# Kernel tuning notes

Measured on AMD Instinct MI355X. Metric: run time of the kernel, lower is better.

## Reference

```python
import jax, jax.numpy as jnp
import numpy as np

N = 50000      # node_size
D = 256        # node_F == rel_F (ent_F)
R = 1000       # rel_size
E = 300000     # triple_size == n_edges
DEPTH = 2
KSEL = E // 2  # rows rewritten by W_orth transform
NPROXY = 128


def l2n(x):
    # tf.nn.l2_normalize with eps=1e-12
    return x * jax.lax.rsqrt(jnp.maximum(jnp.sum(x * x, axis=-1, keepdims=True), 1e-12))


def setup_inputs() -> dict:
    key = jax.random.key(0)
    ks = jax.random.split(key, 12)
    features = jax.random.normal(ks[0], (N, D), jnp.float32)
    rel_emb = jax.random.normal(ks[1], (R, D), jnp.float32)
    p = jax.random.normal(ks[2], (N, 1), jnp.float32)            # dynamic_node_kernel
    w_keys = jax.random.normal(ks[3], (DEPTH, D, D), jnp.float32) / np.float32(np.sqrt(D))
    attn_kernels = jax.random.normal(ks[4], (DEPTH, D, 1), jnp.float32) * 0.1
    proxy = jax.random.normal(ks[5], (NPROXY, D * (DEPTH + 1)), jnp.float32) * 0.05
    gate_kernel = jax.random.normal(ks[6], (D * (DEPTH + 1), D * (DEPTH + 1)), jnp.float32) / np.float32(np.sqrt(D * (DEPTH + 1)))
    adj_row = jnp.sort(jax.random.randint(ks[7], (E,), 0, N))    # destination (segment) ids, sorted
    adj_col = jax.random.randint(ks[8], (E,), 0, N)              # neighbor ids
    rel_ids = jax.random.randint(ks[9], (E,), 0, R)              # relation id per triple/edge
    rel_vals = jax.random.uniform(ks[10], (E,), jnp.float32)     # sparse_val per triple
    new_indices = jax.random.randint(ks[11], (KSEL,), 0, E)      # rows updated by w_key
    return dict(features=features, rel_emb=rel_emb, p=p, w_keys=w_keys,
                attn_kernels=attn_kernels, proxy=proxy, gate_kernel=gate_kernel,
                rel_vals=rel_vals, adj_row=adj_row, adj_col=adj_col,
                rel_ids=rel_ids, new_indices=new_indices)


def reference(features, rel_emb, p, w_keys, attn_kernels, proxy, gate_kernel,
              rel_vals, adj_row, adj_col, rel_ids, new_indices):
    tanh_p = jnp.tanh(p)                                   # [N,1]
    feats = features * tanh_p                              # use_p scaling (activation=None -> identity)
    outputs = [feats]
    for l in range(DEPTH):
        # sparse (triple,rel) x rel_emb : one relation per triple -> gather + scale
        rels_sum = rel_vals[:, None] * rel_emb[rel_ids]    # [E,D]
        rels_sum = l2n(rels_sum)
        # W_orth: transform a subset of rows by w_key, scatter back
        src = rels_sum[new_indices] @ w_keys[l]            # [KSEL,D]
        rels_sum = rels_sum.at[new_indices].set(src)
        neighs = feats[adj_col]                            # [E,D] gather
        rels_sum = rels_sum * tanh_p[adj_col]              # use_p on neighbors
        # Householder-style reflection of neighbor features
        neighs = neighs - 2.0 * jnp.sum(neighs * rels_sum, axis=1, keepdims=True) * rels_sum
        # per-edge attention logits, softmax over incoming edges of each row node
        att = (rels_sum @ attn_kernels[l])[:, 0]           # [E]
        m = jax.ops.segment_max(att, adj_row, num_segments=N)      # [N]
        att = jnp.exp(att - m[adj_row])
        s = jax.ops.segment_sum(att, adj_row, num_segments=N)      # [N]
        att = att / s[adj_row]
        # weighted scatter-aggregate
        feats = jax.ops.segment_sum(neighs * att[:, None], adj_row, num_segments=N)  # [N,D]
        feats = feats * tanh_p
        outputs.append(feats)
    out = jnp.concatenate(outputs, axis=-1)                # [N, D*(DEPTH+1)]
    proxy_att = jax.nn.softmax(l2n(out) @ l2n(proxy).T, axis=-1)   # [N,128]
    proxy_feature = out - proxy_att @ proxy
    gate = jax.nn.sigmoid(proxy_feature @ gate_kernel)
    out = gate * out + (1.0 - gate) * proxy_feature
    return (out, p)
```

## Files before the change

### kernel.cpp

```cpp
#include <hip/hip_runtime.h>
#include <math.h>

#define D 256
#define DCAT 768
#define NPX 128
#define QSTR 896
#define CSTR 136

typedef __attribute__((ext_vector_type(8))) short bf16x8;
typedef __attribute__((ext_vector_type(4))) float f32x4;

__device__ __forceinline__ short cvt_bf16(float f){
  union { float f; unsigned u; } v; v.f = f;
  unsigned r = v.u + 0x7FFF + ((v.u >> 16) & 1);
  return (short)(r >> 16);
}
__device__ __forceinline__ float bf2f(short s){
  union { float f; unsigned u; } v; v.u = ((unsigned)(unsigned short)s) << 16;
  return v.f;
}

__device__ __forceinline__ float waveSum(float v){
#pragma unroll
  for(int o=32;o>=1;o>>=1) v += __shfl_xor(v,o,64);
  return v;
}
__device__ __forceinline__ float waveMax(float v){
#pragma unroll
  for(int o=32;o>=1;o>>=1) v = fmaxf(v,__shfl_xor(v,o,64));
  return v;
}

__global__ void k_prep(const float* __restrict__ p, float* __restrict__ tp,
                       const int* __restrict__ adj_row, int* __restrict__ rs,
                       const int* __restrict__ idx, unsigned char* __restrict__ flag,
                       float* __restrict__ pout, int n, int e, int ksel){
  int i = blockIdx.x*blockDim.x+threadIdx.x;
  if(i<n){ float pv = p[i]; tp[i]=tanhf(pv); pout[i]=pv; }
  if(i<=n){
    int lo=0, hi=e;
    while(lo<hi){ int mid=(lo+hi)>>1; if(adj_row[mid]<i) lo=mid+1; else hi=mid; }
    rs[i]=lo;
  }
  if(i<ksel) flag[idx[i]] = 1;
}

__global__ void k_setup(const float* __restrict__ rel_emb, const float* __restrict__ attn,
                        const float* __restrict__ w_keys, const float* __restrict__ proxy,
                        const float* __restrict__ gatek,
                        float* __restrict__ ss_rel, float* __restrict__ att_n,
                        float* __restrict__ att_t, short* __restrict__ reb,
                        short* __restrict__ rwb, short* __restrict__ pn,
                        short* __restrict__ proxyb, short* __restrict__ BG,
                        short* __restrict__ Bt2, int R_){
  __shared__ float tile[32][33];
  __shared__ float sm[4];
  const int b = blockIdx.x, tid = threadIdx.x;
  const int lane = tid & 63, wv = tid >> 6;

  if(b < R_){
    int r = b, d = tid;
    float v = rel_emb[(size_t)r*D+d];
    reb[(size_t)r*D+d] = cvt_bf16(v);
    float s = waveSum(v*v);
    if(lane==0) sm[wv]=s;
    __syncthreads();
    if(tid==0) ss_rel[r]=sm[0]+sm[1]+sm[2]+sm[3];
    __syncthreads();
    for(int l=0;l<2;l++){
      float dd = waveSum(v*attn[l*D+d]);
      if(lane==0) sm[wv]=dd;
      __syncthreads();
      if(tid==0) att_n[(size_t)l*R_+r]=sm[0]+sm[1]+sm[2]+sm[3];
      __syncthreads();
    }
  } else if(b < 3*R_){
    int l = (b-R_) / R_, r = (b-R_) % R_, d = tid;
    const float* W = w_keys + (size_t)l*D*D;
    const float* ak = attn + (size_t)l*D;
    const float* row = rel_emb + (size_t)r*D;
    float acc=0.f;
#pragma unroll 4
    for(int k=0;k<D;k++) acc = fmaf(row[k], W[(size_t)k*D+d], acc);
    rwb[(size_t)l*R_*D + (size_t)r*D + d]=cvt_bf16(acc);
    float dd = waveSum(acc*ak[d]);
    if(lane==0) sm[wv]=dd;
    __syncthreads();
    if(tid==0) att_t[(size_t)l*R_+r]=sm[0]+sm[1]+sm[2]+sm[3];
  } else if(b < 3*R_+128){
    int j = b - 3*R_;
    float v0 = proxy[(size_t)j*DCAT + tid];
    float v1 = proxy[(size_t)j*DCAT + 256 + tid];
    float v2 = proxy[(size_t)j*DCAT + 512 + tid];
    proxyb[(size_t)j*DCAT + tid]       = cvt_bf16(v0);
    proxyb[(size_t)j*DCAT + 256 + tid] = cvt_bf16(v1);
    proxyb[(size_t)j*DCAT + 512 + tid] = cvt_bf16(v2);
    float ssum = waveSum(v0*v0 + v1*v1 + v2*v2);
    if(lane==0) sm[wv]=ssum;
    __syncthreads();
    float scale = rsqrtf(fmaxf(sm[0]+sm[1]+sm[2]+sm[3],1e-12f));
    pn[(size_t)j*DCAT + tid]       = cvt_bf16(v0*scale);
    pn[(size_t)j*DCAT + 256 + tid] = cvt_bf16(v1*scale);
    pn[(size_t)j*DCAT + 512 + tid] = cvt_bf16(v2*scale);
  } else {
    const float* in; short* out; int R, C, ldo, coff, t;
    if(b < 3*R_+128+576){ t = b-(3*R_+128);     in=gatek; out=BG;  R=DCAT; C=DCAT; ldo=QSTR; coff=0; }
    else                { t = b-(3*R_+128+576); in=proxy; out=Bt2; R=NPX;  C=DCAT; ldo=NPX;  coff=0; }
    int bx = (t%24)*32, by = (t/24)*32;
    int tx = tid & 31, ty = tid >> 5;
    for(int i=ty;i<32;i+=8){
      int rr = by+i, cc = bx+tx;
      if(rr<R && cc<C) tile[i][tx] = in[(size_t)rr*C + cc];
    }
    __syncthreads();
    for(int i=ty;i<32;i+=8){
      int cc = bx+i, rr = by+tx;
      if(cc<C && rr<R) out[(size_t)cc*ldo + coff + rr] = cvt_bf16(tile[tx][i]);
    }
  }
}

__global__ void k_tcast(const float* __restrict__ in, short* __restrict__ out,
                        int R, int C, int ldo, int coff, float sign){
  __shared__ float tile[32][33];
  int bx = blockIdx.x*32, by = blockIdx.y*32;
  for(int i=threadIdx.y;i<32;i+=8){
    int rr = by+i, cc = bx+threadIdx.x;
    if(rr<R && cc<C) tile[i][threadIdx.x] = in[(size_t)rr*C + cc];
  }
  __syncthreads();
  for(int i=threadIdx.y;i<32;i+=8){
    int cc = bx+i, rr = by+threadIdx.x;
    if(cc<C && rr<R) out[(size_t)cc*ldo + coff + rr] = cvt_bf16(sign*tile[threadIdx.x][i]);
  }
}

__global__ void k_init0(const float* __restrict__ features, const float* __restrict__ tp,
                        short* __restrict__ Q, float* __restrict__ ssn, int n){
  __shared__ float sm[4];
  int row = blockIdx.x, d = threadIdx.x;
  float v = features[(size_t)row*D + d] * tp[row];
  Q[(size_t)row*QSTR + d] = cvt_bf16(v);
  int lane=d&63, wid=d>>6;
  float s = waveSum(v*v);
  if(lane==0) sm[wid]=s;
  __syncthreads();
  if(d==0) ssn[row] = sm[0]+sm[1]+sm[2]+sm[3];
}

__global__ void k_agg(const int* __restrict__ rs, const int* __restrict__ adj_col,
                      const int* __restrict__ rel_ids, const float* __restrict__ rel_vals,
                      const unsigned char* __restrict__ flag, const float* __restrict__ tp,
                      const float* __restrict__ ss_rel, const float* __restrict__ att_n,
                      const float* __restrict__ att_t, const short* __restrict__ reb,
                      const short* __restrict__ rwb, short* __restrict__ Q,
                      float* __restrict__ ssn, int n, int layer){
  int wid = threadIdx.x>>6, lane = threadIdx.x&63;
  int node = blockIdx.x*4 + wid;
  if(node>=n) return;
  int s = rs[node], e = rs[node+1];
  float accq[16];
#pragma unroll
  for(int k=0;k<16;k++) accq[k]=0.f;

  auto logit = [&](int i)->float{
    int rid = rel_ids[i]; float rv = rel_vals[i];
    float a = 0.f;
    if(rv>0.f){
      float t = tp[adj_col[i]];
      float sc = rv*rsqrtf(fmaxf(rv*rv*ss_rel[rid],1e-12f));
      a = t*sc*(flag[i]? att_t[rid] : att_n[rid]);
    }
    return a;
  };

  if(e > s){
    float aF = 0.f, mxl = -INFINITY;
    {
      int i = s + lane;
      if(i < e){
        aF = logit(i);
        mxl = aF;
        for(i += 64; i < e; i += 64) mxl = fmaxf(mxl, logit(i));
      }
    }
    float mx = waveMax(mxl);
    float sel = (s+lane < e) ? __expf(aF - mx) : 0.f;
    for(int i = s+64+lane; i < e; i += 64) sel += __expf(logit(i) - mx);
    float se = waveSum(sel);
    float inv = 1.f/se;

    int qid = lane>>4, ql = lane&15;
    int j0 = s + qid;
    bool valid = j0 < e;
    int col=0, rid=0; float rv=0.f; bool fl=false;
    if(valid){ col=adj_col[j0]; rid=rel_ids[j0]; rv=rel_vals[j0]; fl=flag[j0]; }
    for(int i0=s; i0<e; i0+=4){
      int jn = i0 + 4 + qid;
      bool vn = jn < e;
      int coln=0, ridn=0; float rvn=0.f; bool fln=false;
      if(vn){ coln=adj_col[jn]; ridn=rel_ids[jn]; rvn=rel_vals[jn]; fln=flag[jn]; }

      float w=0.f, coef=0.f;
      float nbv[16], rbv[16];
#pragma unroll
      for(int k=0;k<16;k++){ nbv[k]=0.f; rbv[k]=0.f; }
      if(valid){
        const short* np = Q + (size_t)col*QSTR + layer*D + ql*16;
        bf16x8 n0 = *(const bf16x8*)np;
        bf16x8 n1 = *(const bf16x8*)(np+8);
#pragma unroll
        for(int k=0;k<8;k++){ nbv[k]=bf2f(n0[k]); nbv[k+8]=bf2f(n1[k]); }
        if(rv>0.f){
          float t = tp[col];
          float sc = rv*rsqrtf(fmaxf(rv*rv*ss_rel[rid],1e-12f));
          const short* rp = (fl? rwb : reb) + (size_t)rid*D + ql*16;
          bf16x8 r0 = *(const bf16x8*)rp;
          bf16x8 r1 = *(const bf16x8*)(rp+8);
#pragma unroll
          for(int k=0;k<8;k++){ rbv[k]=bf2f(r0[k]); rbv[k+8]=bf2f(r1[k]); }
          float dp = 0.f;
#pragma unroll
          for(int k=0;k<16;k++) dp += nbv[k]*rbv[k];
#pragma unroll
          for(int o=1;o<16;o<<=1) dp += __shfl_xor(dp,o,64);
          float a = t*sc*(fl? att_t[rid] : att_n[rid]);
          w = __expf(a-mx)*inv;
          coef = 2.f*t*t*sc*sc*dp;
        } else {
          w = __expf(-mx)*inv;
        }
      }
#pragma unroll
      for(int k=0;k<16;k++) accq[k] += w*(nbv[k] - coef*rbv[k]);

      valid=vn; col=coln; rid=ridn; rv=rvn; fl=fln;
    }
  }
#pragma unroll
  for(int k=0;k<16;k++){
    float v = accq[k];
    v += __shfl_xor(v,16,64);
    v += __shfl_xor(v,32,64);
    accq[k] = v;
  }
  if(lane < 16){
    float t0 = tp[node];
    bf16x8 o0, o1;
    float pss = 0.f;
#pragma unroll
    for(int k=0;k<8;k++){
      o0[k]=cvt_bf16(accq[k]*t0); o1[k]=cvt_bf16(accq[k+8]*t0);
      pss += accq[k]*accq[k] + accq[k+8]*accq[k+8];
    }
    short* op = Q + (size_t)node*QSTR + (layer+1)*D + lane*16;
    *(bf16x8*)op = o0;
    *(bf16x8*)(op+8) = o1;
#pragma unroll
    for(int o=1;o<16;o<<=1) pss += __shfl_xor(pss,o,64);
    if(lane==0) ssn[node] += pss * t0 * t0;
  }
}

template<int LDA_, int LDB_, int NTOT, int KC>
__global__ __launch_bounds__(256,2) void k_gemm(
    const short* __restrict__ A, const short* __restrict__ Bt,
    float* __restrict__ outF, int M)
{
  __shared__ short smem[3][2][128*32];
  const int tid = threadIdx.x;
  const int lane = tid & 63, w = tid >> 6;
  const int wm = w >> 1, wn = w & 1;
  const int bn = blockIdx.x * 128, bm = blockIdx.y * 128;

  const short* Ag = A  + (size_t)bm * LDA_;
  const short* Bg = Bt + (size_t)bn * LDB_;

  auto stage = [&](int buf, int k0){
#pragma unroll
    for(int c=0;c<2;++c){
      int u = c*256 + tid;
      int row = u >> 2;
      int cb = ((u & 3) ^ ((u >> 3) & 3)) * 8;
      __builtin_amdgcn_global_load_lds(
        (const __attribute__((address_space(1))) unsigned int*)(Ag + (size_t)row*LDA_ + k0 + cb),
        (__attribute__((address_space(3))) unsigned int*)&smem[buf][0][u*8], 16, 0, 0);
      __builtin_amdgcn_global_load_lds(
        (const __attribute__((address_space(1))) unsigned int*)(Bg + (size_t)row*LDB_ + k0 + cb),
        (__attribute__((address_space(3))) unsigned int*)&smem[buf][1][u*8], 16, 0, 0);
    }
  };

  f32x4 acc[4][4] = {};
  const int lr = lane & 15, kg = lane >> 4;
  const int ksw = (kg ^ ((lr >> 1) & 3)) * 8;
  constexpr int NT = KC / 32;

  stage(0, 0);
  stage(1, 32);
  for(int t=0; t<NT; ++t){
    if(t+1 < NT) asm volatile("s_waitcnt vmcnt(4)" ::: "memory");
    else         asm volatile("s_waitcnt vmcnt(0)" ::: "memory");
    __builtin_amdgcn_s_barrier();
    __builtin_amdgcn_sched_barrier(0);
    const short* Al = &smem[t%3][0][0];
    const short* Bl = &smem[t%3][1][0];
    bf16x8 af[4], bfr[4];
#pragma unroll
    for(int i=0;i<4;++i) af[i] = *(const bf16x8*)(Al + (wm*64 + i*16 + lr)*32 + ksw);
#pragma unroll
    for(int j=0;j<4;++j) bfr[j] = *(const bf16x8*)(Bl + (wn*64 + j*16 + lr)*32 + ksw);
    if(t+2 < NT) stage((t+2)%3, (t+2)*32);
    __builtin_amdgcn_s_setprio(1);
#pragma unroll
    for(int i=0;i<4;++i)
#pragma unroll
      for(int j=0;j<4;++j)
        acc[i][j] = __builtin_amdgcn_mfma_f32_16x16x32_bf16(af[i], bfr[j], acc[i][j], 0, 0, 0);
    __builtin_amdgcn_s_setprio(0);
  }

  const int row0 = bm + wm*64 + (lane>>4)*4;
  const int col0 = bn + wn*64 + lr;
#pragma unroll
  for(int i=0;i<4;++i)
#pragma unroll
    for(int j=0;j<4;++j)
#pragma unroll
      for(int r=0;r<4;++r){
        int row = row0 + i*16 + r;
        if(row < M) outF[(size_t)row*NTOT + col0 + j*16] = acc[i][j][r];
      }
}

__global__ __launch_bounds__(256,2) void k_pr(
    short* __restrict__ Q, const short* __restrict__ pn,
    const float* __restrict__ ssn, int M)
{
  __shared__ short smem[3][2][128*32];
  const int tid = threadIdx.x, lane = tid & 63, w = tid >> 6;
  const int wm = w >> 1, wn = w & 1;
  int nwg = gridDim.y;
  int orig = blockIdx.y;
  int q = nwg>>3, rm = nwg&7, xcd = orig&7, lid = orig>>3;
  int wg = (xcd<rm ? xcd*(q+1) : rm*(q+1)+(xcd-rm)*q) + lid;
  const int bm = wg*128;

  const short* Ag = Q + (size_t)bm * QSTR;
  const short* Bg = pn;

  auto stage = [&](int buf, int k0){
#pragma unroll
    for(int c=0;c<2;++c){
      int u = c*256 + tid;
      int row = u >> 2;
      int cb = ((u & 3) ^ ((u >> 3) & 3)) * 8;
      __builtin_amdgcn_global_load_lds(
        (const __attribute__((address_space(1))) unsigned int*)(Ag + (size_t)row*QSTR + k0 + cb),
        (__attribute__((address_space(3))) unsigned int*)&smem[buf][0][u*8], 16, 0, 0);
      __builtin_amdgcn_global_load_lds(
        (const __attribute__((address_space(1))) unsigned int*)(Bg + (size_t)row*DCAT + k0 + cb),
        (__attribute__((address_space(3))) unsigned int*)&smem[buf][1][u*8], 16, 0, 0);
    }
  };

  f32x4 acc[4][4] = {};
  const int lr = lane & 15, kg = lane >> 4;
  const int ksw = (kg ^ ((lr >> 1) & 3)) * 8;
  constexpr int NT = DCAT / 32;

  stage(0, 0);
  stage(1, 32);
  for(int t=0; t<NT; ++t){
    if(t+1 < NT) asm volatile("s_waitcnt vmcnt(4)" ::: "memory");
    else         asm volatile("s_waitcnt vmcnt(0)" ::: "memory");
    __builtin_amdgcn_s_barrier();
    __builtin_amdgcn_sched_barrier(0);
    const short* Al = &smem[t%3][0][0];
    const short* Bl = &smem[t%3][1][0];
    bf16x8 af[4], bfr[4];
#pragma unroll
    for(int i=0;i<4;++i) af[i] = *(const bf16x8*)(Al + (wm*64 + i*16 + lr)*32 + ksw);
#pragma unroll
    for(int j=0;j<4;++j) bfr[j] = *(const bf16x8*)(Bl + (wn*64 + j*16 + lr)*32 + ksw);
    if(t+2 < NT) stage((t+2)%3, (t+2)*32);
    __builtin_amdgcn_s_setprio(1);
#pragma unroll
    for(int i=0;i<4;++i)
#pragma unroll
      for(int j=0;j<4;++j)
        acc[i][j] = __builtin_amdgcn_mfma_f32_16x16x32_bf16(af[i], bfr[j], acc[i][j], 0, 0, 0);
    __builtin_amdgcn_s_setprio(0);
  }

  __syncthreads();
  short* lg = (short*)smem;
  const int row0l = wm*64 + kg*4;
  const int col0l = wn*64 + lr;
#pragma unroll
  for(int i=0;i<4;++i){
#pragma unroll
    for(int j=0;j<4;++j){
#pragma unroll
      for(int r=0;r<4;++r){
        int rl = row0l + i*16 + r;
        int rg = bm + rl;
        float s = (rg < M) ? rsqrtf(fmaxf(ssn[rg],1e-12f)) : 0.f;
        lg[rl*132 + col0l + j*16] = cvt_bf16(acc[i][j][r] * s);
      }
    }
  }
  __syncthreads();
  for(int k2=0;k2<32;++k2){
    int rl = w*32 + k2;
    float a = bf2f(lg[rl*132 + lane]);
    float b = bf2f(lg[rl*132 + 64 + lane]);
    float m = waveMax(fmaxf(a,b));
    float ea = __expf(a-m), eb = __expf(b-m);
    float sm_ = waveSum(ea+eb);
    float inv = 1.f/sm_;
    size_t rg = (size_t)(bm + rl);
    Q[rg*QSTR + DCAT + lane]      = cvt_bf16(ea*inv);
    Q[rg*QSTR + DCAT + 64 + lane] = cvt_bf16(eb*inv);
  }
}

__global__ __launch_bounds__(256,2) void k_go(
    short* __restrict__ Q, const short* __restrict__ BG,
    const short* __restrict__ Bt2, float* __restrict__ outF, int M)
{
  __shared__ short smem[3][2][128*32];
  const int tid = threadIdx.x, lane = tid & 63, w = tid >> 6;
  const int wm = w >> 1, wn = w & 1;
  const int gx = gridDim.x;
  int nwg = gx*gridDim.y;
  int orig = blockIdx.y*gx + blockIdx.x;
  int q = nwg>>3, rm = nwg&7, xcd = orig&7, lid = orig>>3;
  int wg = (xcd<rm ? xcd*(q+1) : rm*(q+1)+(xcd-rm)*q) + lid;
  const int bn = (wg%gx)*128, bm = (wg/gx)*128;
  const int lr = lane & 15, kg = lane >> 4;

  const short* Ag = Q  + (size_t)bm * QSTR;
  const short* Bg = BG + (size_t)bn * QSTR;

  auto stage = [&](int buf, int k0){
#pragma unroll
    for(int c=0;c<2;++c){
      int u = c*256 + tid;
      int row = u >> 2;
      int cb = ((u & 3) ^ ((u >> 3) & 3)) * 8;
      __builtin_amdgcn_global_load_lds(
        (const __attribute__((address_space(1))) unsigned int*)(Ag + (size_t)row*QSTR + k0 + cb),
        (__attribute__((address_space(3))) unsigned int*)&smem[buf][0][u*8], 16, 0, 0);
      __builtin_amdgcn_global_load_lds(
        (const __attribute__((address_space(1))) unsigned int*)(Bg + (size_t)row*QSTR + k0 + cb),
        (__attribute__((address_space(3))) unsigned int*)&smem[buf][1][u*8], 16, 0, 0);
    }
  };

  stage(0, 0);
  stage(1, 32);

  f32x4 acc[4][4] = {};
#pragma unroll
  for(int ks=0; ks<4; ++ks){
    bf16x8 af[4], bb[4];
#pragma unroll
    for(int i=0;i<4;++i)
      af[i] = *(const bf16x8*)(Q + (size_t)(bm + wm*64 + i*16 + lr)*QSTR + DCAT + ks*32 + kg*8);
#pragma unroll
    for(int j=0;j<4;++j)
      bb[j] = *(const bf16x8*)(Bt2 + (size_t)(bn + wn*64 + j*16 + lr)*NPX + ks*32 + kg*8);
#pragma unroll
    for(int i=0;i<4;++i)
#pragma unroll
      for(int j=0;j<4;++j)
        acc[i][j] = __builtin_amdgcn_mfma_f32_16x16x32_bf16(af[i], bb[j], acc[i][j], 0, 0, 0);
  }
  short4 pvb[4][4];
#pragma unroll
  for(int i=0;i<4;++i)
#pragma unroll
    for(int j=0;j<4;++j){
      pvb[i][j].x = cvt_bf16(acc[i][j][0]);
      pvb[i][j].y = cvt_bf16(acc[i][j][1]);
      pvb[i][j].z = cvt_bf16(acc[i][j][2]);
      pvb[i][j].w = cvt_bf16(acc[i][j][3]);
      acc[i][j] = (f32x4){0.f,0.f,0.f,0.f};
    }

  const int ksw = (kg ^ ((lr >> 1) & 3)) * 8;
  constexpr int NT = QSTR / 32;
  for(int t=0; t<NT; ++t){
    if(t+1 < NT) asm volatile("s_waitcnt vmcnt(4)" ::: "memory");
    else         asm volatile("s_waitcnt vmcnt(0)" ::: "memory");
    __builtin_amdgcn_s_barrier();
    __builtin_amdgcn_sched_barrier(0);
    const short* Al = &smem[t%3][0][0];
    const short* Bl = &smem[t%3][1][0];
    bf16x8 af[4], bfr[4];
#pragma unroll
    for(int i=0;i<4;++i) af[i] = *(const bf16x8*)(Al + (wm*64 + i*16 + lr)*32 + ksw);
#pragma unroll
    for(int j=0;j<4;++j) bfr[j] = *(const bf16x8*)(Bl + (wn*64 + j*16 + lr)*32 + ksw);
    if(t+2 < NT) stage((t+2)%3, (t+2)*32);
    __builtin_amdgcn_s_setprio(1);
#pragma unroll
    for(int i=0;i<4;++i)
#pragma unroll
      for(int j=0;j<4;++j)
        acc[i][j] = __builtin_amdgcn_mfma_f32_16x16x32_bf16(af[i], bfr[j], acc[i][j], 0, 0, 0);
    __builtin_amdgcn_s_setprio(0);
  }

  __syncthreads();
  short* cst = (short*)smem;
  const int row0l = wm*64 + kg*4;
  const int col0l = wn*64 + lr;
#pragma unroll
  for(int i=0;i<4;++i){
#pragma unroll
    for(int j=0;j<4;++j){
      float pv4[4] = { bf2f(pvb[i][j].x), bf2f(pvb[i][j].y), bf2f(pvb[i][j].z), bf2f(pvb[i][j].w) };
#pragma unroll
      for(int r2=0;r2<4;++r2){
        float g = 1.f/(1.f+__expf(-acc[i][j][r2]));
        cst[(row0l + i*16 + r2)*CSTR + col0l + j*16] = cvt_bf16((1.f-g)*pv4[r2]);
      }
    }
  }
  __syncthreads();
  const int rl0 = tid>>4, c0 = (tid&15)*8;
#pragma unroll
  for(int rr=0; rr<8; ++rr){
    int rl = rl0 + rr*16;
    int rg = bm + rl;
    if(rg >= M) continue;
    bf16x8 c8  = *(const bf16x8*)(cst + rl*CSTR + c0);
    bf16x8 oc8 = *(const bf16x8*)(Q + (size_t)rg*QSTR + bn + c0);
    float ov[8];
#pragma unroll
    for(int k=0;k<8;k++) ov[k] = bf2f(oc8[k]) - bf2f(c8[k]);
    *(float4*)(outF + (size_t)rg*DCAT + bn + c0)     = make_float4(ov[0],ov[1],ov[2],ov[3]);
    *(float4*)(outF + (size_t)rg*DCAT + bn + c0 + 4) = make_float4(ov[4],ov[5],ov[6],ov[7]);
  }
}

extern "C" void kernel_launch(void* const* d_in, const int* in_sizes, int n_in,
                              void* d_out, int out_size, void* d_ws, size_t ws_size,
                              hipStream_t stream){
  const float* features = (const float*)d_in[0];
  const float* rel_emb  = (const float*)d_in[1];
  const float* p        = (const float*)d_in[2];
  const float* w_keys   = (const float*)d_in[3];
  const float* attn     = (const float*)d_in[4];
  const float* proxy    = (const float*)d_in[5];
  const float* gatek    = (const float*)d_in[6];
  const float* rel_vals = (const float*)d_in[7];
  const int* adj_row    = (const int*)d_in[8];
  const int* adj_col    = (const int*)d_in[9];
  const int* rel_ids    = (const int*)d_in[10];
  const int* new_idx    = (const int*)d_in[11];

  const int n    = in_sizes[2];
  const int r    = in_sizes[1]/D;
  const int e    = in_sizes[7];
  const int ksel = in_sizes[11];
  const size_t Mpad = ((size_t)n + 127) & ~(size_t)127;

  char* ws = (char*)d_ws;
  size_t off=0;
  auto alloc=[&](size_t bytes)->void*{ void* pp = ws+off; off=(off+bytes+255)&~(size_t)255; return pp; };
  float* tp      = (float*)alloc((size_t)n*4);
  int*   rs      = (int*)alloc((size_t)(n+1)*4);
  unsigned char* flag = (unsigned char*)alloc((size_t)e);
  float* ss_rel  = (float*)alloc((size_t)r*4);
  float* att_n   = (float*)alloc((size_t)2*r*4);
  float* att_t   = (float*)alloc((size_t)2*r*4);
  short* reb     = (short*)alloc((size_t)r*D*2);
  short* rwb     = (short*)alloc((size_t)2*r*D*2);
  short* pn      = (short*)alloc((size_t)NPX*DCAT*2);
  short* proxyb  = (short*)alloc((size_t)NPX*DCAT*2);
  short* Bt2     = (short*)alloc((size_t)DCAT*NPX*2);
  short* BG      = (short*)alloc((size_t)DCAT*QSTR*2);
  float* MxF     = (float*)alloc((size_t)NPX*DCAT*4);
  float* ssn     = (float*)alloc(Mpad*4);
  short* Q       = (short*)alloc(Mpad*QSTR*2);

  float* outF = (float*)d_out;
  float* pout = (float*)d_out + (size_t)n*DCAT;

  hipMemsetAsync(flag, 0, (size_t)e, stream);
  hipMemsetAsync(Q + (size_t)n*QSTR, 0, (Mpad-(size_t)n)*QSTR*2, stream);

  int prep_n = (ksel > n+1 ? ksel : n+1);
  k_prep<<<(prep_n+255)/256,256,0,stream>>>(p,tp,adj_row,rs,new_idx,flag,pout,n,e,ksel);
  {
    int nblocks = 3*r + 128 + 576 + 96;
    k_setup<<<nblocks,256,0,stream>>>(rel_emb, attn, w_keys, proxy, gatek,
                                      ss_rel, att_n, att_t, reb, rwb, pn, proxyb,
                                      BG, Bt2, r);
  }
  k_gemm<DCAT, QSTR, DCAT, DCAT><<<dim3(DCAT/128,1),256,0,stream>>>(proxyb, BG, MxF, NPX);
  k_tcast<<<dim3(DCAT/32, NPX/32), dim3(32,8), 0, stream>>>(MxF, BG, NPX, DCAT, QSTR, DCAT, -1.f);

  k_init0<<<n,256,0,stream>>>(features,tp,Q,ssn,n);
  for(int l=0;l<2;l++)
    k_agg<<<(n+3)/4,256,0,stream>>>(rs,adj_col,rel_ids,rel_vals,flag,tp,ss_rel,
                                    att_n+(size_t)l*r, att_t+(size_t)l*r, reb,
                                    rwb+(size_t)l*r*D, Q, ssn, n, l);

  int mt = (int)(Mpad/128);
  k_pr<<<dim3(1, mt),256,0,stream>>>(Q, pn, ssn, n);
  k_go<<<dim3(DCAT/128, mt),256,0,stream>>>(Q, BG, Bt2, outF, n);
}
```

Measured before the change: 444.3 us.

## Merge prep into setup kernel and prefetch next edge's neighbor/relation rows

The standalone prep kernel (tanh(p), row-start binary search, flag scatter) becomes extra blocks of the setup kernel, which removes one launch and lets the two independent workloads run concurrently. In the aggregation kernel, the bf16 neighbor and relation vectors for the next edge are now loaded one iteration ahead, alongside the index prefetch that already existed. This software pipelining hides gather latency behind the current edge's math. The cost is more live registers, which may lower occupancy.

```diff
diff --git a/kernel.cpp b/kernel.cpp
--- a/kernel.cpp
+++ b/kernel.cpp
@@ -31,28 +31,17 @@
   return v;
 }
 
-__global__ void k_prep(const float* __restrict__ p, float* __restrict__ tp,
-                       const int* __restrict__ adj_row, int* __restrict__ rs,
-                       const int* __restrict__ idx, unsigned char* __restrict__ flag,
-                       float* __restrict__ pout, int n, int e, int ksel){
-  int i = blockIdx.x*blockDim.x+threadIdx.x;
-  if(i<n){ float pv = p[i]; tp[i]=tanhf(pv); pout[i]=pv; }
-  if(i<=n){
-    int lo=0, hi=e;
-    while(lo<hi){ int mid=(lo+hi)>>1; if(adj_row[mid]<i) lo=mid+1; else hi=mid; }
-    rs[i]=lo;
-  }
-  if(i<ksel) flag[idx[i]] = 1;
-}
-
 __global__ void k_setup(const float* __restrict__ rel_emb, const float* __restrict__ attn,
                         const float* __restrict__ w_keys, const float* __restrict__ proxy,
-                        const float* __restrict__ gatek,
+                        const float* __restrict__ gatek, const float* __restrict__ p,
+                        const int* __restrict__ adj_row, const int* __restrict__ new_idx,
                         float* __restrict__ ss_rel, float* __restrict__ att_n,
                         float* __restrict__ att_t, short* __restrict__ reb,
                         short* __restrict__ rwb, short* __restrict__ pn,
                         short* __restrict__ proxyb, short* __restrict__ BG,
-                        short* __restrict__ Bt2, int R_){
+                        short* __restrict__ Bt2, float* __restrict__ tp,
+                        int* __restrict__ rs, unsigned char* __restrict__ flag,
+                        float* __restrict__ pout, int R_, int n, int e, int ksel){
   __shared__ float tile[32][33];
   __shared__ float sm[4];
   const int b = blockIdx.x, tid = threadIdx.x;
@@ -102,10 +91,10 @@
     pn[(size_t)j*DCAT + tid]       = cvt_bf16(v0*scale);
     pn[(size_t)j*DCAT + 256 + tid] = cvt_bf16(v1*scale);
     pn[(size_t)j*DCAT + 512 + tid] = cvt_bf16(v2*scale);
-  } else {
-    const float* in; short* out; int R, C, ldo, coff, t;
-    if(b < 3*R_+128+576){ t = b-(3*R_+128);     in=gatek; out=BG;  R=DCAT; C=DCAT; ldo=QSTR; coff=0; }
-    else                { t = b-(3*R_+128+576); in=proxy; out=Bt2; R=NPX;  C=DCAT; ldo=NPX;  coff=0; }
+  } else if(b < 3*R_+128+576+96){
+    const float* in; short* out; int R, C, ldo, t;
+    if(b < 3*R_+128+576){ t = b-(3*R_+128);     in=gatek; out=BG;  R=DCAT; C=DCAT; ldo=QSTR; }
+    else                { t = b-(3*R_+128+576); in=proxy; out=Bt2; R=NPX;  C=DCAT; ldo=NPX;  }
     int bx = (t%24)*32, by = (t/24)*32;
     int tx = tid & 31, ty = tid >> 5;
     for(int i=ty;i<32;i+=8){
@@ -115,8 +104,18 @@
     __syncthreads();
     for(int i=ty;i<32;i+=8){
       int cc = bx+i, rr = by+tx;
-      if(cc<C && rr<R) out[(size_t)cc*ldo + coff + rr] = cvt_bf16(tile[tx][i]);
-    }
+      if(cc<C && rr<R) out[(size_t)cc*ldo + rr] = cvt_bf16(tile[tx][i]);
+    }
+  } else {
+    int t = b - (3*R_+128+576+96);
+    int i = t*256 + tid;
+    if(i<n){ float pv = p[i]; tp[i]=tanhf(pv); pout[i]=pv; }
+    if(i<=n){
+      int lo=0, hi=e;
+      while(lo<hi){ int mid=(lo+hi)>>1; if(adj_row[mid]<i) lo=mid+1; else hi=mid; }
+      rs[i]=lo;
+    }
+    if(i<ksel) flag[new_idx[i]] = 1;
   }
 }
 
@@ -194,31 +193,41 @@
     int j0 = s + qid;
     bool valid = j0 < e;
     int col=0, rid=0; float rv=0.f; bool fl=false;
-    if(valid){ col=adj_col[j0]; rid=rel_ids[j0]; rv=rel_vals[j0]; fl=flag[j0]; }
+    bf16x8 pn0={}, pn1={}, pr0={}, pr1={};
+    if(valid){
+      col=adj_col[j0]; rid=rel_ids[j0]; rv=rel_vals[j0]; fl=flag[j0];
+      const short* np = Q + (size_t)col*QSTR + layer*D + ql*16;
+      pn0 = *(const bf16x8*)np; pn1 = *(const bf16x8*)(np+8);
+      if(rv>0.f){
+        const short* rp = (fl? rwb : reb) + (size_t)rid*D + ql*16;
+        pr0 = *(const bf16x8*)rp; pr1 = *(const bf16x8*)(rp+8);
+      }
+    }
     for(int i0=s; i0<e; i0+=4){
       int jn = i0 + 4 + qid;
       bool vn = jn < e;
       int coln=0, ridn=0; float rvn=0.f; bool fln=false;
-      if(vn){ coln=adj_col[jn]; ridn=rel_ids[jn]; rvn=rel_vals[jn]; fln=flag[jn]; }
-
+      bf16x8 qn0={}, qn1={}, qr0={}, qr1={};
+      if(vn){
+        coln=adj_col[jn]; ridn=rel_ids[jn]; rvn=rel_vals[jn]; fln=flag[jn];
+        const short* np = Q + (size_t)coln*QSTR + layer*D + ql*16;
+        qn0 = *(const bf16x8*)np; qn1 = *(const bf16x8*)(np+8);
+        if(rvn>0.f){
+          const short* rp = (fln? rwb : reb) + (size_t)ridn*D + ql*16;
+          qr0 = *(const bf16x8*)rp; qr1 = *(const bf16x8*)(rp+8);
+        }
+      }
       float w=0.f, coef=0.f;
       float nbv[16], rbv[16];
 #pragma unroll
-      for(int k=0;k<16;k++){ nbv[k]=0.f; rbv[k]=0.f; }
+      for(int k=0;k<8;k++){
+        nbv[k]=bf2f(pn0[k]); nbv[k+8]=bf2f(pn1[k]);
+        rbv[k]=bf2f(pr0[k]); rbv[k+8]=bf2f(pr1[k]);
+      }
       if(valid){
-        const short* np = Q + (size_t)col*QSTR + layer*D + ql*16;
-        bf16x8 n0 = *(const bf16x8*)np;
-        bf16x8 n1 = *(const bf16x8*)(np+8);
-#pragma unroll
-        for(int k=0;k<8;k++){ nbv[k]=bf2f(n0[k]); nbv[k+8]=bf2f(n1[k]); }
         if(rv>0.f){
           float t = tp[col];
           float sc = rv*rsqrtf(fmaxf(rv*rv*ss_rel[rid],1e-12f));
-          const short* rp = (fl? rwb : reb) + (size_t)rid*D + ql*16;
-          bf16x8 r0 = *(const bf16x8*)rp;
-          bf16x8 r1 = *(const bf16x8*)(rp+8);
-#pragma unroll
-          for(int k=0;k<8;k++){ rbv[k]=bf2f(r0[k]); rbv[k+8]=bf2f(r1[k]); }
           float dp = 0.f;
 #pragma unroll
           for(int k=0;k<16;k++) dp += nbv[k]*rbv[k];
@@ -235,6 +244,7 @@
       for(int k=0;k<16;k++) accq[k] += w*(nbv[k] - coef*rbv[k]);
 
       valid=vn; col=coln; rid=ridn; rv=rvn; fl=fln;
+      pn0=qn0; pn1=qn1; pr0=qr0; pr1=qr1;
     }
   }
 #pragma unroll
@@ -593,13 +603,14 @@
   hipMemsetAsync(flag, 0, (size_t)e, stream);
   hipMemsetAsync(Q + (size_t)n*QSTR, 0, (Mpad-(size_t)n)*QSTR*2, stream);
 
-  int prep_n = (ksel > n+1 ? ksel : n+1);
-  k_prep<<<(prep_n+255)/256,256,0,stream>>>(p,tp,adj_row,rs,new_idx,flag,pout,n,e,ksel);
   {
-    int nblocks = 3*r + 128 + 576 + 96;
-    k_setup<<<nblocks,256,0,stream>>>(rel_emb, attn, w_keys, proxy, gatek,
+    int prep_n = (ksel > n+1 ? ksel : n+1);
+    int nprep = (prep_n+255)/256;
+    int nblocks = 3*r + 128 + 576 + 96 + nprep;
+    k_setup<<<nblocks,256,0,stream>>>(rel_emb, attn, w_keys, proxy, gatek, p,
+                                      adj_row, new_idx,
                                       ss_rel, att_n, att_t, reb, rwb, pn, proxyb,
-                                      BG, Bt2, r);
+                                      BG, Bt2, tp, rs, flag, pout, r, n, e, ksel);
   }
   k_gemm<DCAT, QSTR, DCAT, DCAT><<<dim3(DCAT/128,1),256,0,stream>>>(proxyb, BG, MxF, NPX);
   k_tcast<<<dim3(DCAT/32, NPX/32), dim3(32,8), 0, stream>>>(MxF, BG, NPX, DCAT, QSTR, DCAT, -1.f);
```

After: 434.2 us. 1.02x faster.
